# Performance work log

Hardware: AMD Instinct MI355X
Metric: run time of the kernel (lower is better)

## Reference

```python
import jax, jax.numpy as jnp
import numpy as np

N = 100000      # nodes
E = 1600000     # edges (avg degree 16)
D_IN, D_H, D_OUT = 100, 256, 47
EPS = 1e-5


def setup_inputs() -> dict:
    key = jax.random.key(0)
    ks = jax.random.split(key, 10)
    w = lambda k, s: jax.random.normal(k, s, jnp.float32) * 0.02
    return {
        "x": jax.random.normal(ks[0], (N, D_IN), jnp.float32),
        "edge_index": jax.random.randint(ks[1], (2, E), 0, N),
        # SAGEConv 0: lin_l (aggregated neighbors, has bias), lin_r (root, no bias)
        "wl0": w(ks[2], (D_IN, D_H)), "wr0": w(ks[3], (D_IN, D_H)), "b0": jnp.zeros((D_H,), jnp.float32),
        "g0": jnp.ones((D_H,), jnp.float32), "be0": jnp.zeros((D_H,), jnp.float32),
        # SAGEConv 1
        "wl1": w(ks[4], (D_H, D_H)), "wr1": w(ks[5], (D_H, D_H)), "b1": jnp.zeros((D_H,), jnp.float32),
        "g1": jnp.ones((D_H,), jnp.float32), "be1": jnp.zeros((D_H,), jnp.float32),
        # SAGEConv 2 (output)
        "wl2": w(ks[6], (D_H, D_OUT)), "wr2": w(ks[7], (D_H, D_OUT)), "b2": jnp.zeros((D_OUT,), jnp.float32),
    }


def _sage_conv(x, src, dst, wl, wr, b):
    # mean aggregation of source-node features onto destination nodes
    agg = jax.ops.segment_sum(x[src], dst, num_segments=N)          # [N, d_in]
    cnt = jax.ops.segment_sum(jnp.ones((src.shape[0],), x.dtype), dst, num_segments=N)
    mean = agg / jnp.maximum(cnt, 1.0)[:, None]                     # 0 in-degree -> 0
    return mean @ wl + x @ wr + b


def _bn(h, gamma, beta):
    m = h.mean(axis=0)
    v = h.var(axis=0)
    return (h - m) * jax.lax.rsqrt(v + EPS) * gamma + beta


def reference(x, edge_index, wl0, wr0, b0, g0, be0, wl1, wr1, b1, g1, be1, wl2, wr2, b2):
    src, dst = edge_index[0], edge_index[1]
    h = jax.nn.relu(_bn(_sage_conv(x, src, dst, wl0, wr0, b0), g0, be0))
    h = jax.nn.relu(_bn(_sage_conv(h, src, dst, wl1, wr1, b1), g1, be1))
    h = _sage_conv(h, src, dst, wl2, wr2, b2)
    return jax.nn.log_softmax(h, axis=1)
```

## Files before the change

kernel.cpp:

```cpp
#include <hip/hip_runtime.h>
#include <hip/hip_bf16.h>
#include <math.h>

#define DEVFN __device__ __forceinline__

typedef unsigned int uint32;
typedef unsigned short ushort_t;

using bf16x8 = __attribute__((ext_vector_type(8))) short;
using f32x4  = __attribute__((ext_vector_type(4))) float;

DEVFN float bf2f(ushort_t u) {
    union { uint32 i; float f; } v; v.i = ((uint32)u) << 16; return v.f;
}
DEVFN ushort_t f2bf(float f) {
    union { float f; uint32 i; } v; v.f = f;
    uint32 u = v.i;
    uint32 r = (u + 0x7FFFu + ((u >> 16) & 1u)) >> 16;
    return (ushort_t)r;
}

DEVFN void gload_lds16(const void* g, void* l) {
    __builtin_amdgcn_global_load_lds(
        (const __attribute__((address_space(1))) void*)g,
        (__attribute__((address_space(3))) void*)l, 16, 0, 0);
}

__global__ void k_cast_x(const float* __restrict__ x, ushort_t* __restrict__ xb, int N) {
    int total = N * 128;
    for (int i = blockIdx.x * blockDim.x + threadIdx.x; i < total; i += gridDim.x * blockDim.x) {
        int col = i & 127, row = i >> 7;
        float v = (col < 100) ? x[row * 100 + col] : 0.f;
        xb[i] = f2bf(v);
    }
}

__global__ void k_cast_w(const float* __restrict__ w, ushort_t* __restrict__ wt,
                         int K, int Nout, int Kp, int Np) {
    int total = Np * Kp;
    for (int i = blockIdx.x * blockDim.x + threadIdx.x; i < total; i += gridDim.x * blockDim.x) {
        int k = i % Kp, n = i / Kp;
        float v = (k < K && n < Nout) ? w[k * Nout + n] : 0.f;
        wt[i] = f2bf(v);
    }
}

__global__ void k_bincount(const int* __restrict__ dst, int E, int CH, int nbins, int nblk,
                           int* __restrict__ binCnt) {
    __shared__ int scnt[128];
    int blk = blockIdx.x, tid = threadIdx.x;
    for (int b = tid; b < 128; b += 256) scnt[b] = 0;
    __syncthreads();
    int e0 = blk * CH, e1 = min(E, e0 + CH);
    for (int i = e0 + tid; i < e1; i += 256)
        atomicAdd(&scnt[dst[i] >> 10], 1);
    __syncthreads();
    for (int b = tid; b < nbins; b += 256) binCnt[b * nblk + blk] = scnt[b];
}

__global__ void k_blocksum(const int* __restrict__ v, int n, int* __restrict__ bsum) {
    __shared__ int s[1024];
    int i = blockIdx.x * 1024 + threadIdx.x;
    s[threadIdx.x] = (i < n) ? v[i] : 0;
    __syncthreads();
    for (int o = 512; o > 0; o >>= 1) {
        if (threadIdx.x < o) s[threadIdx.x] += s[threadIdx.x + o];
        __syncthreads();
    }
    if (threadIdx.x == 0) bsum[blockIdx.x] = s[0];
}

__global__ void k_scanb(int* __restrict__ bsum, int NB) {
    if (blockIdx.x == 0 && threadIdx.x == 0) {
        int acc = 0;
        for (int i = 0; i < NB; ++i) { int v = bsum[i]; bsum[i] = acc; acc += v; }
    }
}

__global__ void k_exscan(const int* __restrict__ v, const int* __restrict__ bsum,
                         int n, int* __restrict__ outOff) {
    __shared__ int s[1024];
    int t = threadIdx.x;
    int i = blockIdx.x * 1024 + t;
    int val = (i < n) ? v[i] : 0;
    s[t] = val;
    __syncthreads();
    for (int o = 1; o < 1024; o <<= 1) {
        int add = (t >= o) ? s[t - o] : 0;
        __syncthreads();
        s[t] += add;
        __syncthreads();
    }
    if (i < n) outOff[i] = s[t] - val + bsum[blockIdx.x];
}

__global__ void k_binscatter(const int* __restrict__ src, const int* __restrict__ dst,
                             int E, int CH, int nbins, int nblk,
                             const int* __restrict__ binOff, int* __restrict__ ebin) {
    __shared__ int scur[128];
    int blk = blockIdx.x, tid = threadIdx.x;
    for (int b = tid; b < nbins; b += 256) scur[b] = binOff[b * nblk + blk];
    __syncthreads();
    int e0 = blk * CH, e1 = min(E, e0 + CH);
    for (int i = e0 + tid; i < e1; i += 256) {
        int d = dst[i];
        int b = d >> 10;
        int pos = atomicAdd(&scur[b], 1);
        ebin[pos] = (src[i] << 10) | (d & 1023);
    }
}

__global__ void k_bincsr(const int* __restrict__ ebin, const int* __restrict__ binOff,
                         int E, int N, int nbins, int nblk,
                         int* __restrict__ offs, int* __restrict__ deg, int* __restrict__ csr) {
    __shared__ int sdeg[1024];
    __shared__ int scur[1024];
    int bin = blockIdx.x, t = threadIdx.x;
    int binStart = binOff[bin * nblk];
    int binEnd = (bin + 1 < nbins) ? binOff[(bin + 1) * nblk] : E;
    sdeg[t] = 0;
    __syncthreads();
    for (int i = binStart + t; i < binEnd; i += 1024)
        atomicAdd(&sdeg[ebin[i] & 1023], 1);
    __syncthreads();
    int v = sdeg[t];
    for (int o = 1; o < 1024; o <<= 1) {
        int add = (t >= o) ? sdeg[t - o] : 0;
        __syncthreads();
        sdeg[t] += add;
        __syncthreads();
    }
    int ex = sdeg[t] - v;
    int node = bin * 1024 + t;
    if (node < N) { offs[node] = binStart + ex; deg[node] = v; }
    scur[t] = ex;
    __syncthreads();
    for (int i = binStart + t; i < binEnd; i += 1024) {
        int e = ebin[i];
        int slot = atomicAdd(&scur[e & 1023], 1);
        csr[binStart + slot] = e >> 10;
    }
}

template <int DIMS, int BATCH>
__global__ void k_agg(const ushort_t* __restrict__ h, const int* __restrict__ offs,
                      const int* __restrict__ deg, const int* __restrict__ csr,
                      int N, ushort_t* __restrict__ mean) {
    constexpr int VPL = DIMS / 64;
    int wid = (blockIdx.x * blockDim.x + threadIdx.x) >> 6;
    int lane = threadIdx.x & 63;
    if (wid >= N) return;
    int off = offs[wid], cnt = deg[wid];
    float acc[VPL] = {};
    const ushort_t* hp = h + (size_t)lane * VPL;
    if (cnt > 0) {
        int idx[BATCH];
#pragma unroll
        for (int u = 0; u < BATCH; ++u) idx[u] = csr[off + min(u, cnt - 1)];
        for (int b = 0; b < cnt; b += BATCH) {
            if constexpr (VPL == 2) {
                uint32 d[BATCH];
#pragma unroll
                for (int u = 0; u < BATCH; ++u)
                    d[u] = *(const uint32*)(hp + (size_t)idx[u] * DIMS);
                int nxt = b + BATCH;
#pragma unroll
                for (int u = 0; u < BATCH; ++u) idx[u] = csr[off + min(nxt + u, cnt - 1)];
#pragma unroll
                for (int u = 0; u < BATCH; ++u) {
                    float w = (b + u < cnt) ? 1.f : 0.f;
                    acc[0] += w * bf2f((ushort_t)(d[u] & 0xffff));
                    acc[1] += w * bf2f((ushort_t)(d[u] >> 16));
                }
            } else {
                uint2 d[BATCH];
#pragma unroll
                for (int u = 0; u < BATCH; ++u)
                    d[u] = *(const uint2*)(hp + (size_t)idx[u] * DIMS);
                int nxt = b + BATCH;
#pragma unroll
                for (int u = 0; u < BATCH; ++u) idx[u] = csr[off + min(nxt + u, cnt - 1)];
#pragma unroll
                for (int u = 0; u < BATCH; ++u) {
                    float w = (b + u < cnt) ? 1.f : 0.f;
                    acc[0] += w * bf2f((ushort_t)(d[u].x & 0xffff));
                    acc[1] += w * bf2f((ushort_t)(d[u].x >> 16));
                    acc[2] += w * bf2f((ushort_t)(d[u].y & 0xffff));
                    acc[3] += w * bf2f((ushort_t)(d[u].y >> 16));
                }
            }
        }
    }
    float inv = 1.f / fmaxf((float)cnt, 1.f);
    if constexpr (VPL == 2) {
        uint32 o = (uint32)f2bf(acc[0] * inv) | ((uint32)f2bf(acc[1] * inv) << 16);
        *(uint32*)(mean + (size_t)wid * DIMS + lane * 2) = o;
    } else {
        uint2 o;
        o.x = (uint32)f2bf(acc[0] * inv) | ((uint32)f2bf(acc[1] * inv) << 16);
        o.y = (uint32)f2bf(acc[2] * inv) | ((uint32)f2bf(acc[3] * inv) << 16);
        *(uint2*)(mean + (size_t)wid * DIMS + lane * 4) = o;
    }
}

template <int BN, int WROWS, int WCOLS, int MODE>
__global__ __launch_bounds__(512) void k_gemm(
    const ushort_t* __restrict__ A1, const ushort_t* __restrict__ B1,
    const ushort_t* __restrict__ A2, const ushort_t* __restrict__ B2,
    int KP, const float* __restrict__ bias,
    ushort_t* __restrict__ out_bf, float* __restrict__ out_f,
    float* __restrict__ stats, int M) {
    constexpr int BM = 128, BK = 64;
    constexpr int WM = BM / WROWS, WN = BN / WCOLS;
    constexpr int M_REP = WM / 16, N_REP = WN / 16;
    constexpr int SIDES = (MODE == 0) ? 2 : 1;
    __shared__ ushort_t Alds[BM * BK];
    __shared__ ushort_t Blds[BN * BK];
    __shared__ float sstat[2][BN];
    const int tid = threadIdx.x, lane = tid & 63, wid = tid >> 6;
    const int wm = wid / WCOLS, wn = wid % WCOLS;
    const int row0 = blockIdx.x * BM;
    if (MODE == 0) {
        for (int i = tid; i < 2 * BN; i += 512) (&sstat[0][0])[i] = 0.f;
    }
    f32x4 acc[M_REP][N_REP] = {};
    for (int side = 0; side < SIDES; ++side) {
        const ushort_t* A = side ? A2 : A1;
        const ushort_t* B = side ? B2 : B1;
        for (int kt = 0; kt < KP; kt += BK) {
            __syncthreads();
#pragma unroll
            for (int i = tid; i < BM * BK / 8; i += 512) {
                int r = i >> 3, c = i & 7;
                int gr = row0 + r;
                if (gr >= M) gr = M - 1;
                gload_lds16(A + (size_t)gr * KP + kt + c * 8, Alds + i * 8);
            }
#pragma unroll
            for (int i = tid; i < BN * BK / 8; i += 512) {
                int r = i >> 3, c = i & 7;
                gload_lds16(B + (size_t)r * KP + kt + c * 8, Blds + i * 8);
            }
            __syncthreads();
            bf16x8 a[2][M_REP], b[2][N_REP];
#pragma unroll
            for (int kk = 0; kk < 2; ++kk) {
#pragma unroll
                for (int m = 0; m < M_REP; ++m)
                    a[kk][m] = *(const bf16x8*)&Alds[(wm * WM + m * 16 + (lane & 15)) * BK + kk * 32 + (lane >> 4) * 8];
#pragma unroll
                for (int n = 0; n < N_REP; ++n)
                    b[kk][n] = *(const bf16x8*)&Blds[(wn * WN + n * 16 + (lane & 15)) * BK + kk * 32 + (lane >> 4) * 8];
            }
#pragma unroll
            for (int kk = 0; kk < 2; ++kk)
#pragma unroll
                for (int m = 0; m < M_REP; ++m)
#pragma unroll
                    for (int n = 0; n < N_REP; ++n)
                        acc[m][n] = __builtin_amdgcn_mfma_f32_16x16x32_bf16(a[kk][m], b[kk][n], acc[m][n], 0, 0, 0);
        }
    }
#pragma unroll
    for (int n = 0; n < N_REP; ++n) {
        int lcol = wn * WN + n * 16 + (lane & 15);
        float s = 0.f, q = 0.f;
#pragma unroll
        for (int m = 0; m < M_REP; ++m) {
#pragma unroll
            for (int r = 0; r < 4; ++r) {
                int row = row0 + wm * WM + m * 16 + (lane >> 4) * 4 + r;
                float v = acc[m][n][r];
                if (row < M) {
                    if (MODE == 0) {
                        out_bf[(size_t)row * 256 + lcol] = f2bf(v);
                        s += v;
                        q += v * v;
                    } else {
                        if (lcol < 64) {
                            out_bf[(size_t)row * 64 + lcol] = f2bf(v);
                        } else {
                            int c = lcol - 64;
                            float bv = (c < 47) ? bias[c] : 0.f;
                            out_f[(size_t)row * 64 + c] = v + bv;
                        }
                    }
                }
            }
        }
        if (MODE == 0) {
            s += __shfl_xor(s, 16); s += __shfl_xor(s, 32);
            q += __shfl_xor(q, 16); q += __shfl_xor(q, 32);
            if (lane < 16) {
                atomicAdd(&sstat[0][lcol], s);
                atomicAdd(&sstat[1][lcol], q);
            }
        }
    }
    if (MODE == 0) {
        __syncthreads();
        for (int i = tid; i < BN; i += 512) {
            atomicAdd(&stats[i], sstat[0][i]);
            atomicAdd(&stats[256 + i], sstat[1][i]);
        }
    }
}

__global__ void k_bnrelu(const ushort_t* __restrict__ h, const float* __restrict__ stats,
                         const float* __restrict__ g, const float* __restrict__ be,
                         int M, ushort_t* __restrict__ out) {
    int c = threadIdx.x;
    float invM = 1.f / (float)M;
    float mean = stats[c] * invM;
    float var = stats[256 + c] * invM - mean * mean;
    float sc = g[c] * rsqrtf(var + 1e-5f);
    float sh = be[c] - mean * sc;
    for (int r = blockIdx.x; r < M; r += gridDim.x) {
        float v = bf2f(h[(size_t)r * 256 + c]) * sc + sh;
        out[(size_t)r * 256 + c] = f2bf(fmaxf(v, 0.f));
    }
}

__global__ void k_agg_lsm(const ushort_t* __restrict__ t2, const float* __restrict__ r2,
                          const int* __restrict__ offs, const int* __restrict__ deg,
                          const int* __restrict__ csr, int N, float* __restrict__ out) {
    constexpr int BATCH = 16;
    int wid = (blockIdx.x * blockDim.x + threadIdx.x) >> 6;
    int lane = threadIdx.x & 63;
    if (wid >= N) return;
    int off = offs[wid], cnt = deg[wid];
    float acc = 0.f;
    const ushort_t* tp = t2 + lane;
    if (cnt > 0) {
        int idx[BATCH];
#pragma unroll
        for (int u = 0; u < BATCH; ++u) idx[u] = csr[off + min(u, cnt - 1)];
        for (int b = 0; b < cnt; b += BATCH) {
            ushort_t d[BATCH];
#pragma unroll
            for (int u = 0; u < BATCH; ++u) d[u] = tp[(size_t)idx[u] * 64];
            int nxt = b + BATCH;
#pragma unroll
            for (int u = 0; u < BATCH; ++u) idx[u] = csr[off + min(nxt + u, cnt - 1)];
#pragma unroll
            for (int u = 0; u < BATCH; ++u) {
                float w = (b + u < cnt) ? 1.f : 0.f;
                acc += w * bf2f(d[u]);
            }
        }
    }
    float v = acc / fmaxf((float)cnt, 1.f) + r2[(size_t)wid * 64 + lane];
    if (lane >= 47) v = -1e30f;
    float m = v;
    for (int o = 32; o > 0; o >>= 1) m = fmaxf(m, __shfl_xor(m, o));
    float e = (lane < 47) ? expf(v - m) : 0.f;
    float sum = e;
    for (int o = 32; o > 0; o >>= 1) sum += __shfl_xor(sum, o);
    if (lane < 47) out[(size_t)wid * 47 + lane] = v - m - logf(sum);
}

extern "C" void kernel_launch(void* const* d_in, const int* in_sizes, int n_in,
                              void* d_out, int out_size, void* d_ws, size_t ws_size,
                              hipStream_t stream) {
    const float* x   = (const float*)d_in[0];
    const int*   ei  = (const int*)d_in[1];
    const float* wl0 = (const float*)d_in[2];
    const float* wr0 = (const float*)d_in[3];
    const float* g0  = (const float*)d_in[5];
    const float* be0 = (const float*)d_in[6];
    const float* wl1 = (const float*)d_in[7];
    const float* wr1 = (const float*)d_in[8];
    const float* g1  = (const float*)d_in[10];
    const float* be1 = (const float*)d_in[11];
    const float* wl2 = (const float*)d_in[12];
    const float* wr2 = (const float*)d_in[13];
    const float* b2  = (const float*)d_in[14];
    float* out = (float*)d_out;

    const int N = in_sizes[0] / 100;
    const int E = in_sizes[1] / 2;
    const int* src = ei;
    const int* dst = ei + E;

    char* p = (char*)d_ws;
    auto alloc = [&](size_t bytes) -> char* {
        char* r = p;
        p += (bytes + 255) & ~(size_t)255;
        return r;
    };
    ushort_t* xb   = (ushort_t*)alloc((size_t)N * 128 * 2);
    ushort_t* hbuf = (ushort_t*)alloc((size_t)N * 256 * 2);
    ushort_t* mean = (ushort_t*)alloc((size_t)N * 256 * 2);
    ushort_t* hpre = (ushort_t*)alloc((size_t)N * 256 * 2);
    int* deg  = (int*)alloc((size_t)N * 4);
    int* offs = (int*)alloc((size_t)N * 4);
    int* csr  = (int*)alloc((size_t)E * 4);
    int* ebin = (int*)alloc((size_t)E * 4);
    const int NBLK = 128;
    const int nbins = (N + 1023) >> 10;
    const int scanN = nbins * NBLK;
    int* binCnt = (int*)alloc((size_t)scanN * 4);
    int* binOff = (int*)alloc((size_t)scanN * 4);
    int* bsum = (int*)alloc(1024 * 4);
    float* stats = (float*)alloc(512 * 4);
    ushort_t* wlt0 = (ushort_t*)alloc(256 * 128 * 2);
    ushort_t* wrt0 = (ushort_t*)alloc(256 * 128 * 2);
    ushort_t* wlt1 = (ushort_t*)alloc(256 * 256 * 2);
    ushort_t* wrt1 = (ushort_t*)alloc(256 * 256 * 2);
    ushort_t* wcat2 = (ushort_t*)alloc(128 * 256 * 2);
    if ((size_t)(p - (char*)d_ws) > ws_size) return;

    ushort_t* t2 = mean;
    float*    r2 = (float*)((char*)mean + (size_t)N * 64 * 2);

    k_cast_x<<<2048, 256, 0, stream>>>(x, xb, N);
    k_cast_w<<<128, 256, 0, stream>>>(wl0, wlt0, 100, 256, 128, 256);
    k_cast_w<<<128, 256, 0, stream>>>(wr0, wrt0, 100, 256, 128, 256);
    k_cast_w<<<128, 256, 0, stream>>>(wl1, wlt1, 256, 256, 256, 256);
    k_cast_w<<<128, 256, 0, stream>>>(wr1, wrt1, 256, 256, 256, 256);
    k_cast_w<<<128, 256, 0, stream>>>(wl2, wcat2, 256, 47, 256, 64);
    k_cast_w<<<128, 256, 0, stream>>>(wr2, wcat2 + 64 * 256, 256, 47, 256, 64);

    const int CH = (E + NBLK - 1) / NBLK;
    k_bincount<<<NBLK, 256, 0, stream>>>(dst, E, CH, nbins, NBLK, binCnt);
    int NB2 = (scanN + 1023) / 1024;
    k_blocksum<<<NB2, 1024, 0, stream>>>(binCnt, scanN, bsum);
    k_scanb<<<1, 64, 0, stream>>>(bsum, NB2);
    k_exscan<<<NB2, 1024, 0, stream>>>(binCnt, bsum, scanN, binOff);
    k_binscatter<<<NBLK, 256, 0, stream>>>(src, dst, E, CH, nbins, NBLK, binOff, ebin);
    k_bincsr<<<nbins, 1024, 0, stream>>>(ebin, binOff, E, N, nbins, NBLK, offs, deg, csr);

    int aggBlocks = (N + 3) / 4;
    int gemmM = (N + 127) / 128;

    k_agg<128, 16><<<aggBlocks, 256, 0, stream>>>(xb, offs, deg, csr, N, mean);
    hipMemsetAsync(stats, 0, 512 * 4, stream);
    k_gemm<256, 2, 4, 0><<<gemmM, 512, 0, stream>>>(
        mean, wlt0, xb, wrt0, 128, nullptr, hpre, nullptr, stats, N);
    k_bnrelu<<<2048, 256, 0, stream>>>(hpre, stats, g0, be0, N, hbuf);

    k_agg<256, 8><<<aggBlocks, 256, 0, stream>>>(hbuf, offs, deg, csr, N, mean);
    hipMemsetAsync(stats, 0, 512 * 4, stream);
    k_gemm<256, 2, 4, 0><<<gemmM, 512, 0, stream>>>(
        mean, wlt1, hbuf, wrt1, 256, nullptr, hpre, nullptr, stats, N);
    k_bnrelu<<<2048, 256, 0, stream>>>(hpre, stats, g1, be1, N, hbuf);

    k_gemm<128, 2, 4, 1><<<gemmM, 512, 0, stream>>>(
        hbuf, wcat2, nullptr, nullptr, 256, b2, t2, r2, nullptr, N);
    k_agg_lsm<<<(N + 3) / 4, 256, 0, stream>>>(t2, r2, offs, deg, csr, N, out);
}
```

Measured before the change: 580.9 us.

## Slice feature dims across blocks in neighbor aggregation and vectorize BN-ReLU

Replaces the one-wave-per-node aggregation with a sliced version. Each block handles a 16-dim slice for a group of nodes, and lanes split the edges and reduce with shuffles. Layer 1 (256 dims) is split into two launches of 8 slices each. The aim is a smaller per-slice working set of gathered rows, so the random gathers hit L2/MALL more often. The cost is more CSR index reads and cross-lane reductions. BN+ReLU is also rewritten to handle 8 channels per thread with 16-byte loads and stores.

```diff
diff --git a/kernel.cpp b/kernel.cpp
--- a/kernel.cpp
+++ b/kernel.cpp
@@ -5,6 +5,7 @@
 #define DEVFN __device__ __forceinline__
 
 typedef unsigned int uint32;
+typedef unsigned long long uint64;
 typedef unsigned short ushort_t;
 
 using bf16x8 = __attribute__((ext_vector_type(8))) short;
@@ -142,64 +143,45 @@
     }
 }
 
-template <int DIMS, int BATCH>
-__global__ void k_agg(const ushort_t* __restrict__ h, const int* __restrict__ offs,
-                      const int* __restrict__ deg, const int* __restrict__ csr,
-                      int N, ushort_t* __restrict__ mean) {
-    constexpr int VPL = DIMS / 64;
-    int wid = (blockIdx.x * blockDim.x + threadIdx.x) >> 6;
-    int lane = threadIdx.x & 63;
-    if (wid >= N) return;
-    int off = offs[wid], cnt = deg[wid];
-    float acc[VPL] = {};
-    const ushort_t* hp = h + (size_t)lane * VPL;
-    if (cnt > 0) {
-        int idx[BATCH];
-#pragma unroll
-        for (int u = 0; u < BATCH; ++u) idx[u] = csr[off + min(u, cnt - 1)];
-        for (int b = 0; b < cnt; b += BATCH) {
-            if constexpr (VPL == 2) {
-                uint32 d[BATCH];
-#pragma unroll
-                for (int u = 0; u < BATCH; ++u)
-                    d[u] = *(const uint32*)(hp + (size_t)idx[u] * DIMS);
-                int nxt = b + BATCH;
-#pragma unroll
-                for (int u = 0; u < BATCH; ++u) idx[u] = csr[off + min(nxt + u, cnt - 1)];
-#pragma unroll
-                for (int u = 0; u < BATCH; ++u) {
-                    float w = (b + u < cnt) ? 1.f : 0.f;
-                    acc[0] += w * bf2f((ushort_t)(d[u] & 0xffff));
-                    acc[1] += w * bf2f((ushort_t)(d[u] >> 16));
-                }
-            } else {
-                uint2 d[BATCH];
-#pragma unroll
-                for (int u = 0; u < BATCH; ++u)
-                    d[u] = *(const uint2*)(hp + (size_t)idx[u] * DIMS);
-                int nxt = b + BATCH;
-#pragma unroll
-                for (int u = 0; u < BATCH; ++u) idx[u] = csr[off + min(nxt + u, cnt - 1)];
-#pragma unroll
-                for (int u = 0; u < BATCH; ++u) {
-                    float w = (b + u < cnt) ? 1.f : 0.f;
-                    acc[0] += w * bf2f((ushort_t)(d[u].x & 0xffff));
-                    acc[1] += w * bf2f((ushort_t)(d[u].x >> 16));
-                    acc[2] += w * bf2f((ushort_t)(d[u].y & 0xffff));
-                    acc[3] += w * bf2f((ushort_t)(d[u].y >> 16));
-                }
-            }
-        }
-    }
-    float inv = 1.f / fmaxf((float)cnt, 1.f);
-    if constexpr (VPL == 2) {
-        uint32 o = (uint32)f2bf(acc[0] * inv) | ((uint32)f2bf(acc[1] * inv) << 16);
-        *(uint32*)(mean + (size_t)wid * DIMS + lane * 2) = o;
-    } else {
-        uint2 o;
-        o.x = (uint32)f2bf(acc[0] * inv) | ((uint32)f2bf(acc[1] * inv) << 16);
-        o.y = (uint32)f2bf(acc[2] * inv) | ((uint32)f2bf(acc[3] * inv) << 16);
-        *(uint2*)(mean + (size_t)wid * DIMS + lane * 4) = o;
+template <int D>
+__global__ __launch_bounds__(256) void k_agg_slice(
+    const ushort_t* __restrict__ h, const int* __restrict__ offs,
+    const int* __restrict__ deg, const int* __restrict__ csr,
+    int N, int slice0, ushort_t* __restrict__ mean) {
+    constexpr int NPW = 8;
+    const int slice = (blockIdx.x & 7) + slice0;
+    const int nb = blockIdx.x >> 3;
+    const int wv = threadIdx.x >> 6, lane = threadIdx.x & 63;
+    const int g = lane >> 2, l = lane & 3;
+    const int dimBase = slice * 16 + l * 4;
+    const ushort_t* hp = h + dimBase;
+    const int node0 = (nb * 4 + wv) * NPW;
+    for (int nn = 0; nn < NPW; ++nn) {
+        int node = node0 + nn;
+        if (node >= N) return;
+        int off = offs[node], cnt = deg[node];
+        float a0 = 0.f, a1 = 0.f, a2 = 0.f, a3 = 0.f;
+        for (int j = g; j < cnt; j += 16) {
+            int idx = __builtin_nontemporal_load(csr + off + j);
+            uint64 d = *(const uint64*)(hp + (size_t)idx * D);
+            a0 += bf2f((ushort_t)(d & 0xffff));
+            a1 += bf2f((ushort_t)((d >> 16) & 0xffff));
+            a2 += bf2f((ushort_t)((d >> 32) & 0xffff));
+            a3 += bf2f((ushort_t)(d >> 48));
+        }
+#pragma unroll
+        for (int o = 4; o <= 32; o <<= 1) {
+            a0 += __shfl_xor(a0, o);
+            a1 += __shfl_xor(a1, o);
+            a2 += __shfl_xor(a2, o);
+            a3 += __shfl_xor(a3, o);
+        }
+        if (g == 0) {
+            float inv = 1.f / fmaxf((float)cnt, 1.f);
+            uint64 o64 = (uint64)((uint32)f2bf(a0 * inv) | ((uint32)f2bf(a1 * inv) << 16))
+                       | ((uint64)((uint32)f2bf(a2 * inv) | ((uint32)f2bf(a3 * inv) << 16)) << 32);
+            __builtin_nontemporal_store(o64, (uint64*)(mean + (size_t)node * D + dimBase));
+        }
     }
 }
 
@@ -309,15 +291,31 @@
 __global__ void k_bnrelu(const ushort_t* __restrict__ h, const float* __restrict__ stats,
                          const float* __restrict__ g, const float* __restrict__ be,
                          int M, ushort_t* __restrict__ out) {
-    int c = threadIdx.x;
+    int t = threadIdx.x;
+    int cg = (t & 31) * 8;
     float invM = 1.f / (float)M;
-    float mean = stats[c] * invM;
-    float var = stats[256 + c] * invM - mean * mean;
-    float sc = g[c] * rsqrtf(var + 1e-5f);
-    float sh = be[c] - mean * sc;
-    for (int r = blockIdx.x; r < M; r += gridDim.x) {
-        float v = bf2f(h[(size_t)r * 256 + c]) * sc + sh;
-        out[(size_t)r * 256 + c] = f2bf(fmaxf(v, 0.f));
+    float sc[8], sh[8];
+#pragma unroll
+    for (int u = 0; u < 8; ++u) {
+        int c = cg + u;
+        float mean = stats[c] * invM;
+        float var = stats[256 + c] * invM - mean * mean;
+        float s = g[c] * rsqrtf(var + 1e-5f);
+        sc[u] = s;
+        sh[u] = be[c] - mean * s;
+    }
+    for (int r = blockIdx.x * 8 + (t >> 5); r < M; r += gridDim.x * 8) {
+        uint4 d = *(const uint4*)(h + (size_t)r * 256 + cg);
+        uint32 dd[4] = {d.x, d.y, d.z, d.w};
+        uint32 w[4];
+#pragma unroll
+        for (int p = 0; p < 4; ++p) {
+            float lo = bf2f((ushort_t)(dd[p] & 0xffff)) * sc[2 * p] + sh[2 * p];
+            float hi = bf2f((ushort_t)(dd[p] >> 16)) * sc[2 * p + 1] + sh[2 * p + 1];
+            w[p] = (uint32)f2bf(fmaxf(lo, 0.f)) | ((uint32)f2bf(fmaxf(hi, 0.f)) << 16);
+        }
+        uint4 o = {w[0], w[1], w[2], w[3]};
+        *(uint4*)(out + (size_t)r * 256 + cg) = o;
     }
 }
 
@@ -430,16 +428,17 @@
     k_binscatter<<<NBLK, 256, 0, stream>>>(src, dst, E, CH, nbins, NBLK, binOff, ebin);
     k_bincsr<<<nbins, 1024, 0, stream>>>(ebin, binOff, E, N, nbins, NBLK, offs, deg, csr);
 
-    int aggBlocks = (N + 3) / 4;
+    const int sliceBlocks = 8 * ((N + 31) / 32);
     int gemmM = (N + 127) / 128;
 
-    k_agg<128, 16><<<aggBlocks, 256, 0, stream>>>(xb, offs, deg, csr, N, mean);
+    k_agg_slice<128><<<sliceBlocks, 256, 0, stream>>>(xb, offs, deg, csr, N, 0, mean);
     hipMemsetAsync(stats, 0, 512 * 4, stream);
     k_gemm<256, 2, 4, 0><<<gemmM, 512, 0, stream>>>(
         mean, wlt0, xb, wrt0, 128, nullptr, hpre, nullptr, stats, N);
     k_bnrelu<<<2048, 256, 0, stream>>>(hpre, stats, g0, be0, N, hbuf);
 
-    k_agg<256, 8><<<aggBlocks, 256, 0, stream>>>(hbuf, offs, deg, csr, N, mean);
+    k_agg_slice<256><<<sliceBlocks, 256, 0, stream>>>(hbuf, offs, deg, csr, N, 0, mean);
+    k_agg_slice<256><<<sliceBlocks, 256, 0, stream>>>(hbuf, offs, deg, csr, N, 8, mean);
     hipMemsetAsync(stats, 0, 512 * 4, stream);
     k_gemm<256, 2, 4, 0><<<gemmM, 512, 0, stream>>>(
         mean, wlt1, hbuf, wrt1, 256, nullptr, hpre, nullptr, stats, N);
```

Result: slower. 1.300 ms (+123.7%).
